# Optimization experiments

Hardware: AMD Instinct MI355X
Metric: run time of the kernel (lower is better)

## Reference

```python
import jax, jax.numpy as jnp
import numpy as np

V, E, H, NLAB, NL = 30000, 512, 256, 20, 2
B, T = 32, 512


def setup_inputs() -> dict:
    key = jax.random.key(0)
    ks = jax.random.split(key, 11)
    s = 0.05
    return {
        "input": jax.random.randint(ks[0], (B, T), 0, V, dtype=jnp.int32),
        "mask": jnp.ones((B, T), dtype=bool),
        "embed_table": jax.random.normal(ks[1], (V, E), jnp.float32) * s,
        "Wih": jax.random.normal(ks[2], (NL, 2, 4 * H, E), jnp.float32) * s,  # layer input dim E == 2H
        "Whh": jax.random.normal(ks[3], (NL, 2, 4 * H, H), jnp.float32) * s,
        "bias": jax.random.normal(ks[4], (NL, 2, 4 * H), jnp.float32) * s,  # b_ih + b_hh fused
        "lin_W": jax.random.normal(ks[5], (NLAB, 2 * H), jnp.float32) * s,
        "lin_b": jax.random.normal(ks[6], (NLAB,), jnp.float32) * s,
        "transitions": jax.random.normal(ks[7], (NLAB, NLAB), jnp.float32) * 0.1,
        "start_trans": jax.random.normal(ks[8], (NLAB,), jnp.float32) * 0.1,
        "end_trans": jax.random.normal(ks[9], (NLAB,), jnp.float32) * 0.1,
    }


def _lstm_dir(x, Wih, Whh, b, reverse):
    # x: [B,T,in] -> hs: [B,T,H]
    pre = jnp.swapaxes(x, 0, 1) @ Wih.T + b  # [T,B,4H] input projection precomputed
    h0 = jnp.zeros((x.shape[0], Whh.shape[1]), x.dtype)

    def step(carry, p):
        h, c = carry
        g = p + h @ Whh.T
        i, f, gg, o = jnp.split(g, 4, axis=-1)  # pytorch gate order i,f,g,o
        i = jax.nn.sigmoid(i); f = jax.nn.sigmoid(f)
        gg = jnp.tanh(gg); o = jax.nn.sigmoid(o)
        c = f * c + i * gg
        h = o * jnp.tanh(c)
        return (h, c), h

    _, hs = jax.lax.scan(step, (h0, h0), pre, reverse=reverse)
    return jnp.swapaxes(hs, 0, 1)


def _bilstm(x, Wih, Whh, bias):
    out = x
    for l in range(Wih.shape[0]):
        f = _lstm_dir(out, Wih[l, 0], Whh[l, 0], bias[l, 0], False)
        bwd = _lstm_dir(out, Wih[l, 1], Whh[l, 1], bias[l, 1], True)
        out = jnp.concatenate([f, bwd], axis=-1)
    return out


def _viterbi(em, mask, trans, start, end):
    # em: [B,T,L], mask: [B,T] (mask[:,0] assumed all True, as torchcrf requires)
    Bz, Tz, Lz = em.shape
    ar = jnp.arange(Lz, dtype=jnp.int32)
    score0 = start[None, :] + em[:, 0]

    def step(score, xs):
        em_t, m_t = xs  # [B,L], [B]
        ns = score[:, :, None] + trans[None] + em_t[:, None, :]  # [B,L_prev,L_cur]
        best = ns.max(axis=1)
        idx = ns.argmax(axis=1).astype(jnp.int32)
        score = jnp.where(m_t[:, None], best, score)
        idx = jnp.where(m_t[:, None], idx, ar[None, :])  # identity bp for padded steps
        return score, idx

    em_tb = jnp.swapaxes(em, 0, 1)
    m_tb = jnp.swapaxes(mask, 0, 1)
    score, hist = jax.lax.scan(step, score0, (em_tb[1:], m_tb[1:]))
    score = score + end[None, :]
    last = jnp.argmax(score, axis=-1).astype(jnp.int32)
    bidx = jnp.arange(Bz)

    def back(tag, bp):
        prev = bp[bidx, tag]
        return prev, prev

    _, prevs = jax.lax.scan(back, last, hist, reverse=True)  # prevs[t] = tag_t for t=0..T-2
    tags = jnp.concatenate([prevs, last[None]], axis=0)  # [T,B]
    return jnp.swapaxes(tags, 0, 1), score.max(axis=-1)


def reference(input, mask, embed_table, Wih, Whh, bias, lin_W, lin_b, transitions, start_trans, end_trans):
    x = embed_table[input]                      # [B,T,E]
    h = _bilstm(x, Wih, Whh, bias)              # [B,T,2H]
    em = h @ lin_W.T + lin_b                    # [B,T,L]
    tags, _ = _viterbi(em, mask, transitions, start_trans, end_trans)
    return tags
```

## Files before the change

### kernel.cpp

```cpp
#include <hip/hip_runtime.h>
#include <math.h>


#define T_SEQ   512
#define BATCH   32
#define HID     256
#define NLAB    20

#define AGENT __HIP_MEMORY_SCOPE_AGENT
#define HB_STRIDE 576
#define HB_LAYER  (64 * HB_STRIDE)

__device__ __forceinline__ float fsig(float x) {
  float e = __builtin_amdgcn_exp2f(-1.44269504088896340736f * x);
  return __builtin_amdgcn_rcpf(1.f + e);
}
__device__ __forceinline__ float ftanh(float x) {
  float e = __builtin_amdgcn_exp2f(2.88539008177792681471f * x);
  return 1.f - 2.f * __builtin_amdgcn_rcpf(e + 1.f);
}
__device__ __forceinline__ float addx1(float x) {
  int p = __builtin_amdgcn_update_dpp(0, __float_as_int(x), 0xB1, 0xF, 0xF, true);
  return x + __int_as_float(p);
}
__device__ __forceinline__ float addx2(float x) {
  int p = __builtin_amdgcn_update_dpp(0, __float_as_int(x), 0x4E, 0xF, 0xF, true);
  return x + __int_as_float(p);
}
__device__ __forceinline__ float addx4h(float x) {
  int p = __builtin_amdgcn_update_dpp(0, __float_as_int(x), 0x141, 0xF, 0xF, true);
  return x + __int_as_float(p);
}

__device__ __forceinline__ void store_l2(unsigned long long* p, unsigned long long v) {
  asm volatile("global_store_dwordx2 %0, %1, off" :: "v"(p), "v"(v) : "memory");
}
__device__ __forceinline__ unsigned long long load_l2(const unsigned long long* p) {
  unsigned long long v;
  asm volatile("global_load_dwordx2 %0, %1, off sc0\n\ts_waitcnt vmcnt(0)"
               : "=v"(v) : "v"(p) : "memory");
  return v;
}

__global__ __launch_bounds__(256) void prep_wih_k(const float* __restrict__ Wih,
                                                  const float* __restrict__ bias,
                                                  float* __restrict__ Wp,
                                                  float* __restrict__ bpp) {
  int idx = blockIdx.x * 256 + threadIdx.x;
  int k4 = idx & 127;
  int n  = (idx >> 7) & 1023;
  int ld = idx >> 17;
  int q = n & 3, j = n >> 2;
  int src = ld * 1024 + q * 256 + j;
  ((float4*)Wp)[idx] = ((const float4*)Wih)[(size_t)src * 128 + k4];
  if (k4 == 0) bpp[ld * 1024 + n] = bias[src];
}

__global__ __launch_bounds__(256) void prep_whh_reg_k(const float* __restrict__ Whh,
                                                      float4* __restrict__ Wreg) {
  int idx = blockIdx.x * 256 + threadIdx.x;
  int t  = idx & 511;
  int i  = (idx >> 9) & 31;
  int bx = (idx >> 14) & 3;
  int ld = idx >> 16;
  int u = bx * 64 + (t >> 3);
  int q = i >> 3, c = i & 7;
  int k = (t & 7) * 32 + c * 4;
  Wreg[idx] = ((const float4*)Whh)[((size_t)(ld * 1024 + q * 256 + u) * 256 + k) >> 2];
}

__global__ __launch_bounds__(256) void zero_hbuf_k(int4* __restrict__ p) {
  p[blockIdx.x * 256 + threadIdx.x] = int4{0, 0, 0, 0};
}

__global__ __launch_bounds__(256) void embed_k(const int* __restrict__ inp,
                                               const float* __restrict__ tab,
                                               float* __restrict__ x) {
  int idx = blockIdx.x * 256 + threadIdx.x;
  int row = idx >> 7, c = idx & 127;
  int tok = inp[row];
  ((float4*)x)[idx] = ((const float4*)tab)[(size_t)tok * 128 + c];
}

#define GBM 128
#define GBN 128
#define GBK 32
__global__ __launch_bounds__(256) void gemm_nt_k(const float* __restrict__ A,
                                                 const float* __restrict__ W,
                                                 const float* __restrict__ bias,
                                                 float* __restrict__ C,
                                                 int M, int N, int K) {
  __shared__ float As[GBK][GBM];
  __shared__ float Ws[GBK][GBN];
  int tid = threadIdx.x;
  int bm = blockIdx.x, bn = blockIdx.y;
  int tm = (tid & 15) * 8, tn = (tid >> 4) * 8;
  int r  = tid >> 1;
  int kq = (tid & 1) * 16;
  const float* Ap = A + (size_t)(bm * GBM + r) * K + kq;
  const float* Wq = W + (size_t)(bn * GBN + r) * K + kq;

  float acc[8][8] = {};
  float4 av[4], wv[4];

#pragma unroll
  for (int j = 0; j < 4; ++j) {
    av[j] = *(const float4*)(Ap + 4 * j);
    wv[j] = *(const float4*)(Wq + 4 * j);
  }

  for (int k0 = 0; k0 < K; k0 += GBK) {
    __syncthreads();
#pragma unroll
    for (int j = 0; j < 4; ++j) {
      float ta[4], tw[4];
      *(float4*)ta = av[j]; *(float4*)tw = wv[j];
#pragma unroll
      for (int e = 0; e < 4; ++e) {
        As[kq + 4 * j + e][r] = ta[e];
        Ws[kq + 4 * j + e][r] = tw[e];
      }
    }
    __syncthreads();
    if (k0 + GBK < K) {
#pragma unroll
      for (int j = 0; j < 4; ++j) {
        av[j] = *(const float4*)(Ap + k0 + GBK + 4 * j);
        wv[j] = *(const float4*)(Wq + k0 + GBK + 4 * j);
      }
    }
#pragma unroll
    for (int kk = 0; kk < GBK; ++kk) {
      float a8[8], b8[8];
      *(float4*)&a8[0] = *(const float4*)&As[kk][tm];
      *(float4*)&a8[4] = *(const float4*)&As[kk][tm + 4];
      *(float4*)&b8[0] = *(const float4*)&Ws[kk][tn];
      *(float4*)&b8[4] = *(const float4*)&Ws[kk][tn + 4];
#pragma unroll
      for (int i = 0; i < 8; ++i)
#pragma unroll
        for (int j = 0; j < 8; ++j)
          acc[i][j] = fmaf(a8[i], b8[j], acc[i][j]);
    }
  }

  int m0 = bm * GBM + tm, n0 = bn * GBN + tn;
  float4 bv0 = *(const float4*)(bias + n0);
  float4 bv1 = *(const float4*)(bias + n0 + 4);
#pragma unroll
  for (int i = 0; i < 8; ++i) {
    float4 o0, o1;
    o0.x = acc[i][0] + bv0.x; o0.y = acc[i][1] + bv0.y;
    o0.z = acc[i][2] + bv0.z; o0.w = acc[i][3] + bv0.w;
    o1.x = acc[i][4] + bv1.x; o1.y = acc[i][5] + bv1.y;
    o1.z = acc[i][6] + bv1.z; o1.w = acc[i][7] + bv1.w;
    *(float4*)&C[(size_t)(m0 + i) * N + n0]     = o0;
    *(float4*)&C[(size_t)(m0 + i) * N + n0 + 4] = o1;
  }
}

__global__ __launch_bounds__(512, 1) void lstm_group_k(const float* __restrict__ pre,
                                                       const float4* __restrict__ WregL,
                                                       unsigned long long* __restrict__ hbufA,
                                                       unsigned long long* __restrict__ hbufB,
                                                       float* __restrict__ Hout) {
  int raw = blockIdx.x;
  int xcd = raw & 7, slot = raw >> 3;
  int g  = xcd * 8 + (slot >> 2);
  int bx = slot & 3;
  int b = g >> 1, d = g & 1;
  int tid = threadIdx.x;
  int kq = tid & 7;
  int uu = tid >> 3;
  int u  = bx * 64 + uu;
  bool lead = (kq == 0);

  __shared__ __align__(16) float hout_s[T_SEQ * 64];
  __shared__ __align__(16) float h_s[2][8 * 36];

  float4 w[32];
  const float4* wp = WregL + ((size_t)(d * 4 + bx) * 32) * 512 + tid;
#pragma unroll
  for (int i = 0; i < 32; ++i) w[i] = wp[i * 512];

  unsigned long long* hbA = hbufA + (size_t)g * HB_STRIDE;
  unsigned long long* hbB = hbufB + (size_t)g * HB_STRIDE;
  const float* preB = pre + (size_t)b * T_SEQ * 2048 + d * 1024 + bx * 256 + 4 * uu;

  float c = 0.f;

  {
    int t = d ? (T_SEQ - 1) : 0;
    float4 g4 = *(const float4*)(preB + (size_t)t * 2048);
    float iv = fsig(g4.x), fv = fsig(g4.y);
    float zv = ftanh(g4.z), ov = fsig(g4.w);
    c = fv * c + iv * zv;
    float hn = ov * ftanh(c);
    if (lead) {
      unsigned long long pv = (1ULL << 32) | (unsigned long long)__float_as_uint(hn);
      store_l2(&hbA[256 + u], pv);
      __hip_atomic_store(&hbB[256 + u], pv, __ATOMIC_RELAXED, AGENT);
      hout_s[t * 64 + uu] = hn;
    }
  }

  for (int s = 1; s < T_SEQ; ++s) {
    int t = d ? (T_SEQ - 1 - s) : s;
    float4 p4 = *(const float4*)(preB + (size_t)t * 2048);

    if (tid < 256) {
      unsigned long long* pa = &hbA[(s & 1) * 256 + tid];
      unsigned long long* pb = &hbB[(s & 1) * 256 + tid];
      unsigned long long v;
      bool got = false;
      for (int tries = 0; tries < 6; ++tries) {
        v = load_l2(pa);
        if (__all((unsigned)(v >> 32) == (unsigned)s)) { got = true; break; }
      }
      if (!got) {
        for (;;) {
          v = __hip_atomic_load(pb, __ATOMIC_RELAXED, AGENT);
          if (__all((unsigned)(v >> 32) == (unsigned)s)) break;
          __builtin_amdgcn_s_sleep(1);
        }
      }
      h_s[s & 1][(tid >> 5) * 36 + (tid & 31)] = __uint_as_float((unsigned)v);
    }
    __syncthreads();

    const float* hk = &h_s[s & 1][kq * 36];
    float4 a0 = {0.f, 0.f, 0.f, 0.f}, a1 = a0, a2 = a0, a3 = a0;
#pragma unroll
    for (int c8 = 0; c8 < 8; ++c8) {
      float4 h4 = *(const float4*)(hk + 4 * c8);
      a0.x = fmaf(w[c8].x,      h4.x, a0.x); a0.y = fmaf(w[c8].y,      h4.y, a0.y);
      a0.z = fmaf(w[c8].z,      h4.z, a0.z); a0.w = fmaf(w[c8].w,      h4.w, a0.w);
      a1.x = fmaf(w[8 + c8].x,  h4.x, a1.x); a1.y = fmaf(w[8 + c8].y,  h4.y, a1.y);
      a1.z = fmaf(w[8 + c8].z,  h4.z, a1.z); a1.w = fmaf(w[8 + c8].w,  h4.w, a1.w);
      a2.x = fmaf(w[16 + c8].x, h4.x, a2.x); a2.y = fmaf(w[16 + c8].y, h4.y, a2.y);
      a2.z = fmaf(w[16 + c8].z, h4.z, a2.z); a2.w = fmaf(w[16 + c8].w, h4.w, a2.w);
      a3.x = fmaf(w[24 + c8].x, h4.x, a3.x); a3.y = fmaf(w[24 + c8].y, h4.y, a3.y);
      a3.z = fmaf(w[24 + c8].z, h4.z, a3.z); a3.w = fmaf(w[24 + c8].w, h4.w, a3.w);
    }
    float gi = (a0.x + a0.y) + (a0.z + a0.w);
    float gf = (a1.x + a1.y) + (a1.z + a1.w);
    float gg = (a2.x + a2.y) + (a2.z + a2.w);
    float go = (a3.x + a3.y) + (a3.z + a3.w);
    gi = addx4h(addx2(addx1(gi))) + p4.x;
    gf = addx4h(addx2(addx1(gf))) + p4.y;
    gg = addx4h(addx2(addx1(gg))) + p4.z;
    go = addx4h(addx2(addx1(go))) + p4.w;

    float iv = fsig(gi), fv = fsig(gf);
    float zv = ftanh(gg), ov = fsig(go);
    c = fv * c + iv * zv;
    float hn = ov * ftanh(c);

    if (lead) {
      if (s < T_SEQ - 1) {
        unsigned long long pv = ((unsigned long long)(unsigned)(s + 1) << 32) |
                                (unsigned long long)__float_as_uint(hn);
        store_l2(&hbA[((s + 1) & 1) * 256 + u], pv);
        __hip_atomic_store(&hbB[((s + 1) & 1) * 256 + u], pv, __ATOMIC_RELAXED, AGENT);
      }
      hout_s[t * 64 + uu] = hn;
    }
  }

  __syncthreads();
  const float4* src = (const float4*)hout_s;
  float4* dst = (float4*)Hout;
#pragma unroll
  for (int i = 0; i < 16; ++i) {
    int idx = i * 512 + tid;
    int t = idx >> 4, c4 = idx & 15;
    dst[((size_t)(b * T_SEQ + t) << 7) + d * 64 + bx * 16 + c4] = src[idx];
  }
}

__global__ __launch_bounds__(256) void linear20_k(const float* __restrict__ H,
                                                  const float* __restrict__ LW,
                                                  const float* __restrict__ lb,
                                                  float* __restrict__ em) {
  __shared__ float hs[8 * 516];
  __shared__ float lws[20 * 516];
  int tid = threadIdx.x;
  int m0 = blockIdx.x * 8;
  const float4* Hp = (const float4*)(H + (size_t)m0 * 512);
  for (int v = tid; v < 1024; v += 256) {
    int rr = v >> 7, cc = v & 127;
    *(float4*)&hs[rr * 516 + cc * 4] = Hp[v];
  }
  for (int v = tid; v < 2560; v += 256) {
    int ll = v >> 7, cc = v & 127;
    *(float4*)&lws[ll * 516 + cc * 4] = ((const float4*)LW)[v];
  }
  __syncthreads();
  if (tid < 160) {
    int rr = tid / 20, ll = tid % 20;
    float acc = 0.f;
    const float* hp = &hs[rr * 516];
    const float* wp = &lws[ll * 516];
#pragma unroll 8
    for (int k = 0; k < 512; ++k) acc += hp[k] * wp[k];
    em[(size_t)(m0 + rr) * 20 + ll] = acc + lb[ll];
  }
}

__global__ __launch_bounds__(640) void viterbi_k(const float* __restrict__ em,
                                                 const float* __restrict__ trans,
                                                 const float* __restrict__ startt,
                                                 const float* __restrict__ endt,
                                                 int* __restrict__ tags) {
  __shared__ float em_s[T_SEQ * NLAB];
  __shared__ float trans_s[NLAB * NLAB];
  __shared__ float score_s[NLAB];
  __shared__ unsigned char bp[(T_SEQ - 1) * NLAB];
  int b = blockIdx.x, tid = threadIdx.x;
  const float4* emb = (const float4*)(em + (size_t)b * T_SEQ * NLAB);
  for (int v = tid; v < T_SEQ * NLAB / 4; v += 640) ((float4*)em_s)[v] = emb[v];
  for (int v = tid; v < NLAB * NLAB; v += 640) trans_s[v] = trans[v];
  if (tid < NLAB) score_s[tid] = startt[tid] + em[(size_t)b * T_SEQ * NLAB + tid];
  __syncthreads();
  int j = tid >> 5;
  int i = tid & 31;
  float tr = (i < NLAB) ? trans_s[i * NLAB + j] : -1e30f;
  for (int t = 1; t < T_SEQ; ++t) {
    float v = (i < NLAB) ? (score_s[i] + tr) : -1e30f;
    int bi = i;
#pragma unroll
    for (int off = 16; off > 0; off >>= 1) {
      float ov = __shfl_down(v, off, 32);
      int oi = __shfl_down(bi, off, 32);
      if (ov > v || (ov == v && oi < bi)) { v = ov; bi = oi; }
    }
    __syncthreads();
    if (i == 0) {
      score_s[j] = v + em_s[t * NLAB + j];
      bp[(t - 1) * NLAB + j] = (unsigned char)bi;
    }
    __syncthreads();
  }
  if (tid == 0) {
    float best = score_s[0] + endt[0]; int cur = 0;
    for (int l = 1; l < NLAB; ++l) {
      float sv = score_s[l] + endt[l];
      if (sv > best) { best = sv; cur = l; }
    }
    int* tb = tags + b * T_SEQ;
    tb[T_SEQ - 1] = cur;
    for (int s2 = T_SEQ - 2; s2 >= 0; --s2) { cur = bp[s2 * NLAB + cur]; tb[s2] = cur; }
  }
}

extern "C" void kernel_launch(void* const* d_in, const int* in_sizes, int n_in,
                              void* d_out, int out_size, void* d_ws, size_t ws_size,
                              hipStream_t stream) {
  const int*   inp   = (const int*)d_in[0];
  const float* tab   = (const float*)d_in[2];
  const float* Wih   = (const float*)d_in[3];
  const float* Whh   = (const float*)d_in[4];
  const float* bias  = (const float*)d_in[5];
  const float* linW  = (const float*)d_in[6];
  const float* linb  = (const float*)d_in[7];
  const float* trans = (const float*)d_in[8];
  const float* stt   = (const float*)d_in[9];
  const float* endt  = (const float*)d_in[10];
  int* tags = (int*)d_out;

  float* ws   = (float*)d_ws;
  float* Wp   = ws;
  float* Wreg = Wp + 2097152;
  float* bpp  = Wreg + 1048576;
  float* x    = bpp + 4096;
  float* H0   = x + 8388608;
  float* pre  = H0 + 8388608;
  float* em   = pre + 33554432;
  unsigned long long* hbufA = (unsigned long long*)em;
  unsigned long long* hbufB = hbufA + 2 * HB_LAYER;

  const float4* WregF4 = (const float4*)Wreg;

  hipLaunchKernelGGL(zero_hbuf_k, dim3(288), dim3(256), 0, stream, (int4*)hbufA);
  hipLaunchKernelGGL(prep_wih_k, dim3(2048), dim3(256), 0, stream, Wih, bias, Wp, bpp);
  hipLaunchKernelGGL(prep_whh_reg_k, dim3(1024), dim3(256), 0, stream, Whh, (float4*)Wreg);
  hipLaunchKernelGGL(embed_k, dim3(8192), dim3(256), 0, stream, inp, tab, x);

  const int M = BATCH * T_SEQ;
  hipLaunchKernelGGL(gemm_nt_k, dim3(M / GBM, 2048 / GBN), dim3(256), 0, stream,
                     x, Wp, bpp, pre, M, 2048, 512);
  hipLaunchKernelGGL(lstm_group_k, dim3(256), dim3(512), 0, stream,
                     pre, WregF4, hbufA, hbufB, H0);
  hipLaunchKernelGGL(gemm_nt_k, dim3(M / GBM, 2048 / GBN), dim3(256), 0, stream,
                     H0, Wp + 2048 * 512, bpp + 2048, pre, M, 2048, 512);
  hipLaunchKernelGGL(lstm_group_k, dim3(256), dim3(512), 0, stream,
                     pre, WregF4 + 2 * 65536, hbufA + HB_LAYER, hbufB + HB_LAYER, x);
  hipLaunchKernelGGL(linear20_k, dim3(M / 8), dim3(256), 0, stream, x, linW, linb, em);
  hipLaunchKernelGGL(viterbi_k, dim3(BATCH), dim3(640), 0, stream, em, trans, stt, endt, tags);
}
```

Before: 2.844 ms.

## Interleave forward and backward LSTM directions within each workgroup

Each workgroup now handles 32 hidden units for both directions of one batch element, where before it handled 64 units of a single direction. It keeps both directions' recurrent weights in registers and alternates polling and compute between them, so one direction's cross-workgroup h exchange latency can overlap with the other's matvec. The reduction now spans 16 lanes and the Whh register layout is reorganised to match. The risk is two barriers per step instead of one, plus serialised polling that may not actually hide latency.

```diff
diff --git a/kernel.cpp b/kernel.cpp
--- a/kernel.cpp
+++ b/kernel.cpp
@@ -29,6 +29,10 @@
 }
 __device__ __forceinline__ float addx4h(float x) {
   int p = __builtin_amdgcn_update_dpp(0, __float_as_int(x), 0x141, 0xF, 0xF, true);
+  return x + __int_as_float(p);
+}
+__device__ __forceinline__ float addx8m(float x) {
+  int p = __builtin_amdgcn_update_dpp(0, __float_as_int(x), 0x140, 0xF, 0xF, true);
   return x + __int_as_float(p);
 }
 
@@ -40,6 +44,28 @@
   asm volatile("global_load_dwordx2 %0, %1, off sc0\n\ts_waitcnt vmcnt(0)"
                : "=v"(v) : "v"(p) : "memory");
   return v;
+}
+__device__ __forceinline__ unsigned long long poll_u64(unsigned long long* fast,
+                                                       unsigned long long* slow,
+                                                       unsigned s) {
+  unsigned long long v;
+  for (int tries = 0; tries < 6; ++tries) {
+    v = load_l2(fast);
+    if (__all((unsigned)(v >> 32) == s)) return v;
+  }
+  for (;;) {
+    v = __hip_atomic_load(slow, __ATOMIC_RELAXED, AGENT);
+    if (__all((unsigned)(v >> 32) == s)) return v;
+    __builtin_amdgcn_s_sleep(1);
+  }
+}
+__device__ __forceinline__ float gdot(const float4* w, int q,
+                                      float4 h0, float4 h1, float4 h2, float4 h3) {
+  float ax = fmaf(w[q*4+0].x, h0.x, fmaf(w[q*4+1].x, h1.x, fmaf(w[q*4+2].x, h2.x, w[q*4+3].x * h3.x)));
+  float ay = fmaf(w[q*4+0].y, h0.y, fmaf(w[q*4+1].y, h1.y, fmaf(w[q*4+2].y, h2.y, w[q*4+3].y * h3.y)));
+  float az = fmaf(w[q*4+0].z, h0.z, fmaf(w[q*4+1].z, h1.z, fmaf(w[q*4+2].z, h2.z, w[q*4+3].z * h3.z)));
+  float aw = fmaf(w[q*4+0].w, h0.w, fmaf(w[q*4+1].w, h1.w, fmaf(w[q*4+2].w, h2.w, w[q*4+3].w * h3.w)));
+  return (ax + ay) + (az + aw);
 }
 
 __global__ __launch_bounds__(256) void prep_wih_k(const float* __restrict__ Wih,
@@ -59,13 +85,13 @@
 __global__ __launch_bounds__(256) void prep_whh_reg_k(const float* __restrict__ Whh,
                                                       float4* __restrict__ Wreg) {
   int idx = blockIdx.x * 256 + threadIdx.x;
-  int t  = idx & 511;
-  int i  = (idx >> 9) & 31;
-  int bx = (idx >> 14) & 3;
-  int ld = idx >> 16;
-  int u = bx * 64 + (t >> 3);
-  int q = i >> 3, c = i & 7;
-  int k = (t & 7) * 32 + c * 4;
+  int t   = idx & 511;
+  int i   = (idx >> 9) & 15;
+  int ub8 = (idx >> 13) & 7;
+  int ld  = idx >> 16;
+  int u = ub8 * 32 + (t >> 4);
+  int q = i >> 2, c = i & 3;
+  int k = (t & 15) * 16 + c * 4;
   Wreg[idx] = ((const float4*)Whh)[((size_t)(ld * 1024 + q * 256 + u) * 256 + k) >> 2];
 }
 
@@ -159,111 +185,133 @@
   }
 }
 
-__global__ __launch_bounds__(512, 1) void lstm_group_k(const float* __restrict__ pre,
-                                                       const float4* __restrict__ WregL,
-                                                       unsigned long long* __restrict__ hbufA,
-                                                       unsigned long long* __restrict__ hbufB,
-                                                       float* __restrict__ Hout) {
+__global__ __launch_bounds__(512, 1) void lstm_pair_k(const float* __restrict__ pre,
+                                                      const float4* __restrict__ WregL,
+                                                      unsigned long long* __restrict__ fastb,
+                                                      unsigned long long* __restrict__ slowb,
+                                                      float* __restrict__ Hout) {
   int raw = blockIdx.x;
   int xcd = raw & 7, slot = raw >> 3;
-  int g  = xcd * 8 + (slot >> 2);
-  int bx = slot & 3;
-  int b = g >> 1, d = g & 1;
+  int p   = xcd * 4 + (slot >> 3);
+  int ub8 = slot & 7;
+  int b = p;
   int tid = threadIdx.x;
-  int kq = tid & 7;
-  int uu = tid >> 3;
-  int u  = bx * 64 + uu;
+  int kq = tid & 15;
+  int uu = tid >> 4;
+  int u  = ub8 * 32 + uu;
   bool lead = (kq == 0);
 
-  __shared__ __align__(16) float hout_s[T_SEQ * 64];
-  __shared__ __align__(16) float h_s[2][8 * 36];
-
-  float4 w[32];
-  const float4* wp = WregL + ((size_t)(d * 4 + bx) * 32) * 512 + tid;
-#pragma unroll
-  for (int i = 0; i < 32; ++i) w[i] = wp[i * 512];
-
-  unsigned long long* hbA = hbufA + (size_t)g * HB_STRIDE;
-  unsigned long long* hbB = hbufB + (size_t)g * HB_STRIDE;
-  const float* preB = pre + (size_t)b * T_SEQ * 2048 + d * 1024 + bx * 256 + 4 * uu;
-
-  float c = 0.f;
-
+  __shared__ __align__(16) float hout_s[2][T_SEQ][32];
+  __shared__ __align__(16) float h_sA[2][16 * 18];
+  __shared__ __align__(16) float h_sB[2][16 * 18];
+
+  float4 w0[16], w1[16];
   {
-    int t = d ? (T_SEQ - 1) : 0;
-    float4 g4 = *(const float4*)(preB + (size_t)t * 2048);
-    float iv = fsig(g4.x), fv = fsig(g4.y);
-    float zv = ftanh(g4.z), ov = fsig(g4.w);
-    c = fv * c + iv * zv;
-    float hn = ov * ftanh(c);
+    const float4* wp0 = WregL + (size_t)ub8 * 8192 + tid;
+    const float4* wp1 = wp0 + 65536;
+#pragma unroll
+    for (int i = 0; i < 16; ++i) { w0[i] = wp0[i * 512]; w1[i] = wp1[i * 512]; }
+  }
+
+  int gA = 2 * b, gB = 2 * b + 1;
+  unsigned long long* fA = fastb + (size_t)gA * HB_STRIDE;
+  unsigned long long* fB = fastb + (size_t)gB * HB_STRIDE;
+  unsigned long long* sA = slowb + (size_t)gA * HB_STRIDE;
+  unsigned long long* sB = slowb + (size_t)gB * HB_STRIDE;
+
+  const float* preP = pre + (size_t)b * T_SEQ * 2048 + ub8 * 128 + 4 * uu;
+
+  float cA = 0.f, cB = 0.f;
+
+  {
+    float4 g4 = *(const float4*)(preP);
+    float iv = fsig(g4.x), fv = fsig(g4.y), zv = ftanh(g4.z), ov = fsig(g4.w);
+    cA = fv * cA + iv * zv;
+    float hn = ov * ftanh(cA);
     if (lead) {
+      hout_s[0][0][uu] = hn;
       unsigned long long pv = (1ULL << 32) | (unsigned long long)__float_as_uint(hn);
-      store_l2(&hbA[256 + u], pv);
-      __hip_atomic_store(&hbB[256 + u], pv, __ATOMIC_RELAXED, AGENT);
-      hout_s[t * 64 + uu] = hn;
+      store_l2(&fA[256 + u], pv);
+      __hip_atomic_store(&sA[256 + u], pv, __ATOMIC_RELAXED, AGENT);
+    }
+    float4 g5 = *(const float4*)(preP + (size_t)(T_SEQ - 1) * 2048 + 1024);
+    float iv2 = fsig(g5.x), fv2 = fsig(g5.y), zv2 = ftanh(g5.z), ov2 = fsig(g5.w);
+    cB = fv2 * cB + iv2 * zv2;
+    float hn2 = ov2 * ftanh(cB);
+    if (lead) {
+      hout_s[1][T_SEQ - 1][uu] = hn2;
+      unsigned long long pv = (1ULL << 32) | (unsigned long long)__float_as_uint(hn2);
+      store_l2(&fB[256 + u], pv);
+      __hip_atomic_store(&sB[256 + u], pv, __ATOMIC_RELAXED, AGENT);
     }
   }
 
   for (int s = 1; s < T_SEQ; ++s) {
-    int t = d ? (T_SEQ - 1 - s) : s;
-    float4 p4 = *(const float4*)(preB + (size_t)t * 2048);
+    int tA = s, tB = T_SEQ - 1 - s;
+    int sl = s & 1;
+    float4 pA = *(const float4*)(preP + (size_t)tA * 2048);
+    float4 pB = *(const float4*)(preP + (size_t)tB * 2048 + 1024);
 
     if (tid < 256) {
-      unsigned long long* pa = &hbA[(s & 1) * 256 + tid];
-      unsigned long long* pb = &hbB[(s & 1) * 256 + tid];
-      unsigned long long v;
-      bool got = false;
-      for (int tries = 0; tries < 6; ++tries) {
-        v = load_l2(pa);
-        if (__all((unsigned)(v >> 32) == (unsigned)s)) { got = true; break; }
-      }
-      if (!got) {
-        for (;;) {
-          v = __hip_atomic_load(pb, __ATOMIC_RELAXED, AGENT);
-          if (__all((unsigned)(v >> 32) == (unsigned)s)) break;
-          __builtin_amdgcn_s_sleep(1);
+      unsigned long long v = poll_u64(&fA[sl * 256 + tid], &sA[sl * 256 + tid], (unsigned)s);
+      h_sA[sl][(tid >> 4) * 18 + (tid & 15)] = __uint_as_float((unsigned)v);
+    }
+    __syncthreads();
+    {
+      const float* hk = &h_sA[sl][kq * 18];
+      float4 h0 = *(const float4*)hk,       h1 = *(const float4*)(hk + 4),
+             h2 = *(const float4*)(hk + 8), h3 = *(const float4*)(hk + 12);
+      float gi = gdot(w0, 0, h0, h1, h2, h3);
+      float gf = gdot(w0, 1, h0, h1, h2, h3);
+      float gg = gdot(w0, 2, h0, h1, h2, h3);
+      float go = gdot(w0, 3, h0, h1, h2, h3);
+      gi = addx8m(addx4h(addx2(addx1(gi)))) + pA.x;
+      gf = addx8m(addx4h(addx2(addx1(gf)))) + pA.y;
+      gg = addx8m(addx4h(addx2(addx1(gg)))) + pA.z;
+      go = addx8m(addx4h(addx2(addx1(go)))) + pA.w;
+      float iv = fsig(gi), fv = fsig(gf), zv = ftanh(gg), ov = fsig(go);
+      cA = fv * cA + iv * zv;
+      float hn = ov * ftanh(cA);
+      if (lead) {
+        hout_s[0][tA][uu] = hn;
+        if (s < T_SEQ - 1) {
+          unsigned long long pv = ((unsigned long long)(unsigned)(s + 1) << 32) |
+                                  (unsigned long long)__float_as_uint(hn);
+          store_l2(&fA[((s + 1) & 1) * 256 + u], pv);
+          __hip_atomic_store(&sA[((s + 1) & 1) * 256 + u], pv, __ATOMIC_RELAXED, AGENT);
         }
       }
-      h_s[s & 1][(tid >> 5) * 36 + (tid & 31)] = __uint_as_float((unsigned)v);
-    }
-    __syncthreads();
-
-    const float* hk = &h_s[s & 1][kq * 36];
-    float4 a0 = {0.f, 0.f, 0.f, 0.f}, a1 = a0, a2 = a0, a3 = a0;
-#pragma unroll
-    for (int c8 = 0; c8 < 8; ++c8) {
-      float4 h4 = *(const float4*)(hk + 4 * c8);
-      a0.x = fmaf(w[c8].x,      h4.x, a0.x); a0.y = fmaf(w[c8].y,      h4.y, a0.y);
-      a0.z = fmaf(w[c8].z,      h4.z, a0.z); a0.w = fmaf(w[c8].w,      h4.w, a0.w);
-      a1.x = fmaf(w[8 + c8].x,  h4.x, a1.x); a1.y = fmaf(w[8 + c8].y,  h4.y, a1.y);
-      a1.z = fmaf(w[8 + c8].z,  h4.z, a1.z); a1.w = fmaf(w[8 + c8].w,  h4.w, a1.w);
-      a2.x = fmaf(w[16 + c8].x, h4.x, a2.x); a2.y = fmaf(w[16 + c8].y, h4.y, a2.y);
-      a2.z = fmaf(w[16 + c8].z, h4.z, a2.z); a2.w = fmaf(w[16 + c8].w, h4.w, a2.w);
-      a3.x = fmaf(w[24 + c8].x, h4.x, a3.x); a3.y = fmaf(w[24 + c8].y, h4.y, a3.y);
-      a3.z = fmaf(w[24 + c8].z, h4.z, a3.z); a3.w = fmaf(w[24 + c8].w, h4.w, a3.w);
-    }
-    float gi = (a0.x + a0.y) + (a0.z + a0.w);
-    float gf = (a1.x + a1.y) + (a1.z + a1.w);
-    float gg = (a2.x + a2.y) + (a2.z + a2.w);
-    float go = (a3.x + a3.y) + (a3.z + a3.w);
-    gi = addx4h(addx2(addx1(gi))) + p4.x;
-    gf = addx4h(addx2(addx1(gf))) + p4.y;
-    gg = addx4h(addx2(addx1(gg))) + p4.z;
-    go = addx4h(addx2(addx1(go))) + p4.w;
-
-    float iv = fsig(gi), fv = fsig(gf);
-    float zv = ftanh(gg), ov = fsig(go);
-    c = fv * c + iv * zv;
-    float hn = ov * ftanh(c);
-
-    if (lead) {
-      if (s < T_SEQ - 1) {
-        unsigned long long pv = ((unsigned long long)(unsigned)(s + 1) << 32) |
-                                (unsigned long long)__float_as_uint(hn);
-        store_l2(&hbA[((s + 1) & 1) * 256 + u], pv);
-        __hip_atomic_store(&hbB[((s + 1) & 1) * 256 + u], pv, __ATOMIC_RELAXED, AGENT);
+    }
+
+    if (tid < 256) {
+      unsigned long long v = poll_u64(&fB[sl * 256 + tid], &sB[sl * 256 + tid], (unsigned)s);
+      h_sB[sl][(tid >> 4) * 18 + (tid & 15)] = __uint_as_float((unsigned)v);
+    }
+    __syncthreads();
+    {
+      const float* hk = &h_sB[sl][kq * 18];
+      float4 h0 = *(const float4*)hk,       h1 = *(const float4*)(hk + 4),
+             h2 = *(const float4*)(hk + 8), h3 = *(const float4*)(hk + 12);
+      float gi = gdot(w1, 0, h0, h1, h2, h3);
+      float gf = gdot(w1, 1, h0, h1, h2, h3);
+      float gg = gdot(w1, 2, h0, h1, h2, h3);
+      float go = gdot(w1, 3, h0, h1, h2, h3);
+      gi = addx8m(addx4h(addx2(addx1(gi)))) + pB.x;
+      gf = addx8m(addx4h(addx2(addx1(gf)))) + pB.y;
+      gg = addx8m(addx4h(addx2(addx1(gg)))) + pB.z;
+      go = addx8m(addx4h(addx2(addx1(go)))) + pB.w;
+      float iv = fsig(gi), fv = fsig(gf), zv = ftanh(gg), ov = fsig(go);
+      cB = fv * cB + iv * zv;
+      float hn = ov * ftanh(cB);
+      if (lead) {
+        hout_s[1][tB][uu] = hn;
+        if (s < T_SEQ - 1) {
+          unsigned long long pv = ((unsigned long long)(unsigned)(s + 1) << 32) |
+                                  (unsigned long long)__float_as_uint(hn);
+          store_l2(&fB[((s + 1) & 1) * 256 + u], pv);
+          __hip_atomic_store(&sB[((s + 1) & 1) * 256 + u], pv, __ATOMIC_RELAXED, AGENT);
+        }
       }
-      hout_s[t * 64 + uu] = hn;
     }
   }
 
@@ -273,8 +321,10 @@
 #pragma unroll
   for (int i = 0; i < 16; ++i) {
     int idx = i * 512 + tid;
-    int t = idx >> 4, c4 = idx & 15;
-    dst[((size_t)(b * T_SEQ + t) << 7) + d * 64 + bx * 16 + c4] = src[idx];
+    int d = idx >> 12;
+    int rem = idx & 4095;
+    int t = rem >> 3, c4 = rem & 7;
+    dst[((size_t)(b * T_SEQ + t) << 7) + d * 64 + ub8 * 8 + c4] = src[idx];
   }
 }
 
@@ -376,12 +426,12 @@
   float* H0   = x + 8388608;
   float* pre  = H0 + 8388608;
   float* em   = pre + 33554432;
-  unsigned long long* hbufA = (unsigned long long*)em;
-  unsigned long long* hbufB = hbufA + 2 * HB_LAYER;
+  unsigned long long* fastb = (unsigned long long*)em;
+  unsigned long long* slowb = fastb + 2 * HB_LAYER;
 
   const float4* WregF4 = (const float4*)Wreg;
 
-  hipLaunchKernelGGL(zero_hbuf_k, dim3(288), dim3(256), 0, stream, (int4*)hbufA);
+  hipLaunchKernelGGL(zero_hbuf_k, dim3(288), dim3(256), 0, stream, (int4*)fastb);
   hipLaunchKernelGGL(prep_wih_k, dim3(2048), dim3(256), 0, stream, Wih, bias, Wp, bpp);
   hipLaunchKernelGGL(prep_whh_reg_k, dim3(1024), dim3(256), 0, stream, Whh, (float4*)Wreg);
   hipLaunchKernelGGL(embed_k, dim3(8192), dim3(256), 0, stream, inp, tab, x);
@@ -389,12 +439,12 @@
   const int M = BATCH * T_SEQ;
   hipLaunchKernelGGL(gemm_nt_k, dim3(M / GBM, 2048 / GBN), dim3(256), 0, stream,
                      x, Wp, bpp, pre, M, 2048, 512);
-  hipLaunchKernelGGL(lstm_group_k, dim3(256), dim3(512), 0, stream,
-                     pre, WregF4, hbufA, hbufB, H0);
+  hipLaunchKernelGGL(lstm_pair_k, dim3(256), dim3(512), 0, stream,
+                     pre, WregF4, fastb, slowb, H0);
   hipLaunchKernelGGL(gemm_nt_k, dim3(M / GBM, 2048 / GBN), dim3(256), 0, stream,
                      H0, Wp + 2048 * 512, bpp + 2048, pre, M, 2048, 512);
-  hipLaunchKernelGGL(lstm_group_k, dim3(256), dim3(512), 0, stream,
-                     pre, WregF4 + 2 * 65536, hbufA + HB_LAYER, hbufB + HB_LAYER, x);
+  hipLaunchKernelGGL(lstm_pair_k, dim3(256), dim3(512), 0, stream,
+                     pre, WregF4 + 131072, fastb + HB_LAYER, slowb + HB_LAYER, x);
   hipLaunchKernelGGL(linear20_k, dim3(M / 8), dim3(256), 0, stream, x, linW, linb, em);
   hipLaunchKernelGGL(viterbi_k, dim3(BATCH), dim3(640), 0, stream, em, trans, stt, endt, tags);
 }
```

After: 5.258 ms. 1.85x slower.

## Enlarge GEMM tile to 256x128 and prefetch next-step preactivations in LSTM

Applied to the files above, without the earlier changes.

The input-projection GEMM tile grows from 128x128 to 256x128, with each thread computing 16x8 outputs. Shared memory gets padded strides and coalesced row-wise global loads, which raises arithmetic intensity per shared load. Separately, the LSTM recurrence loads the next timestep's precomputed gate inputs one step ahead, taking that global load latency off the serial per-step critical path. The bigger tile uses more registers and halves the grid in M, which may reduce occupancy.

```diff
diff --git a/kernel.cpp b/kernel.cpp
--- a/kernel.cpp
+++ b/kernel.cpp
@@ -82,81 +82,101 @@
   ((float4*)x)[idx] = ((const float4*)tab)[(size_t)tok * 128 + c];
 }
 
-#define GBM 128
+#define GBM 256
 #define GBN 128
 #define GBK 32
-__global__ __launch_bounds__(256) void gemm_nt_k(const float* __restrict__ A,
-                                                 const float* __restrict__ W,
-                                                 const float* __restrict__ bias,
-                                                 float* __restrict__ C,
-                                                 int M, int N, int K) {
-  __shared__ float As[GBK][GBM];
-  __shared__ float Ws[GBK][GBN];
+#define LDA 258
+#define LDB 130
+__global__ __launch_bounds__(256, 2) void gemm_nt_k(const float* __restrict__ A,
+                                                    const float* __restrict__ W,
+                                                    const float* __restrict__ bias,
+                                                    float* __restrict__ C,
+                                                    int M, int N, int K) {
+  __shared__ float As[GBK * LDA];
+  __shared__ float Ws[GBK * LDB];
   int tid = threadIdx.x;
   int bm = blockIdx.x, bn = blockIdx.y;
-  int tm = (tid & 15) * 8, tn = (tid >> 4) * 8;
-  int r  = tid >> 1;
-  int kq = (tid & 1) * 16;
-  const float* Ap = A + (size_t)(bm * GBM + r) * K + kq;
-  const float* Wq = W + (size_t)(bn * GBN + r) * K + kq;
-
-  float acc[8][8] = {};
-  float4 av[4], wv[4];
-
-#pragma unroll
-  for (int j = 0; j < 4; ++j) {
-    av[j] = *(const float4*)(Ap + 4 * j);
-    wv[j] = *(const float4*)(Wq + 4 * j);
+  int tm = (tid & 15) * 4;
+  int tn = (tid >> 4) * 8;
+  const float* Ap = A + (size_t)(bm * GBM) * K;
+  const float* Wq = W + (size_t)(bn * GBN) * K;
+
+  float acc[16][8] = {};
+  float4 avr[8], wvr[4];
+
+#pragma unroll
+  for (int i = 0; i < 8; ++i) {
+    int v = i * 256 + tid;
+    avr[i] = *(const float4*)(Ap + (size_t)(v >> 3) * K + (v & 7) * 4);
+  }
+#pragma unroll
+  for (int i = 0; i < 4; ++i) {
+    int v = i * 256 + tid;
+    wvr[i] = *(const float4*)(Wq + (size_t)(v >> 3) * K + (v & 7) * 4);
   }
 
   for (int k0 = 0; k0 < K; k0 += GBK) {
     __syncthreads();
 #pragma unroll
-    for (int j = 0; j < 4; ++j) {
-      float ta[4], tw[4];
-      *(float4*)ta = av[j]; *(float4*)tw = wv[j];
-#pragma unroll
-      for (int e = 0; e < 4; ++e) {
-        As[kq + 4 * j + e][r] = ta[e];
-        Ws[kq + 4 * j + e][r] = tw[e];
-      }
+    for (int i = 0; i < 8; ++i) {
+      int v = i * 256 + tid, r = v >> 3, kc = (v & 7) * 4;
+      float tmp[4]; *(float4*)tmp = avr[i];
+#pragma unroll
+      for (int e = 0; e < 4; ++e) As[(kc + e) * LDA + r] = tmp[e];
+    }
+#pragma unroll
+    for (int i = 0; i < 4; ++i) {
+      int v = i * 256 + tid, r = v >> 3, kc = (v & 7) * 4;
+      float tmp[4]; *(float4*)tmp = wvr[i];
+#pragma unroll
+      for (int e = 0; e < 4; ++e) Ws[(kc + e) * LDB + r] = tmp[e];
     }
     __syncthreads();
     if (k0 + GBK < K) {
 #pragma unroll
-      for (int j = 0; j < 4; ++j) {
-        av[j] = *(const float4*)(Ap + k0 + GBK + 4 * j);
-        wv[j] = *(const float4*)(Wq + k0 + GBK + 4 * j);
+      for (int i = 0; i < 8; ++i) {
+        int v = i * 256 + tid;
+        avr[i] = *(const float4*)(Ap + (size_t)(v >> 3) * K + k0 + GBK + (v & 7) * 4);
       }
+#pragma unroll
+      for (int i = 0; i < 4; ++i) {
+        int v = i * 256 + tid;
+        wvr[i] = *(const float4*)(Wq + (size_t)(v >> 3) * K + k0 + GBK + (v & 7) * 4);
+      }
     }
 #pragma unroll
     for (int kk = 0; kk < GBK; ++kk) {
-      float a8[8], b8[8];
-      *(float4*)&a8[0] = *(const float4*)&As[kk][tm];
-      *(float4*)&a8[4] = *(const float4*)&As[kk][tm + 4];
-      *(float4*)&b8[0] = *(const float4*)&Ws[kk][tn];
-      *(float4*)&b8[4] = *(const float4*)&Ws[kk][tn + 4];
-#pragma unroll
-      for (int i = 0; i < 8; ++i)
+      float a16[16], b8[8];
+#pragma unroll
+      for (int g = 0; g < 4; ++g)
+        *(float4*)&a16[4 * g] = *(const float4*)&As[kk * LDA + tm + 64 * g];
+      *(float4*)&b8[0] = *(const float4*)&Ws[kk * LDB + tn];
+      *(float4*)&b8[4] = *(const float4*)&Ws[kk * LDB + tn + 4];
+#pragma unroll
+      for (int i = 0; i < 16; ++i)
 #pragma unroll
         for (int j = 0; j < 8; ++j)
-          acc[i][j] = fmaf(a8[i], b8[j], acc[i][j]);
-    }
-  }
-
-  int m0 = bm * GBM + tm, n0 = bn * GBN + tn;
+          acc[i][j] = fmaf(a16[i], b8[j], acc[i][j]);
+    }
+  }
+
+  int n0 = bn * GBN + tn;
   float4 bv0 = *(const float4*)(bias + n0);
   float4 bv1 = *(const float4*)(bias + n0 + 4);
 #pragma unroll
-  for (int i = 0; i < 8; ++i) {
-    float4 o0, o1;
-    o0.x = acc[i][0] + bv0.x; o0.y = acc[i][1] + bv0.y;
-    o0.z = acc[i][2] + bv0.z; o0.w = acc[i][3] + bv0.w;
-    o1.x = acc[i][4] + bv1.x; o1.y = acc[i][5] + bv1.y;
-    o1.z = acc[i][6] + bv1.z; o1.w = acc[i][7] + bv1.w;
-    *(float4*)&C[(size_t)(m0 + i) * N + n0]     = o0;
-    *(float4*)&C[(size_t)(m0 + i) * N + n0 + 4] = o1;
-  }
+  for (int g = 0; g < 4; ++g)
+#pragma unroll
+    for (int e = 0; e < 4; ++e) {
+      int i = g * 4 + e;
+      int row = bm * GBM + tm + 64 * g + e;
+      float4 o0, o1;
+      o0.x = acc[i][0] + bv0.x; o0.y = acc[i][1] + bv0.y;
+      o0.z = acc[i][2] + bv0.z; o0.w = acc[i][3] + bv0.w;
+      o1.x = acc[i][4] + bv1.x; o1.y = acc[i][5] + bv1.y;
+      o1.z = acc[i][6] + bv1.z; o1.w = acc[i][7] + bv1.w;
+      *(float4*)&C[(size_t)row * N + n0]     = o0;
+      *(float4*)&C[(size_t)row * N + n0 + 4] = o1;
+    }
 }
 
 __global__ __launch_bounds__(512, 1) void lstm_group_k(const float* __restrict__ pre,
@@ -204,9 +224,10 @@
     }
   }
 
+  float4 p_cur = *(const float4*)(preB + (size_t)(d ? (T_SEQ - 2) : 1) * 2048);
+
   for (int s = 1; s < T_SEQ; ++s) {
     int t = d ? (T_SEQ - 1 - s) : s;
-    float4 p4 = *(const float4*)(preB + (size_t)t * 2048);
 
     if (tid < 256) {
       unsigned long long* pa = &hbA[(s & 1) * 256 + tid];
@@ -228,6 +249,9 @@
     }
     __syncthreads();
 
+    int snx = (s + 1 < T_SEQ) ? s + 1 : s;
+    float4 p_nxt = *(const float4*)(preB + (size_t)(d ? (T_SEQ - 1 - snx) : snx) * 2048);
+
     const float* hk = &h_s[s & 1][kq * 36];
     float4 a0 = {0.f, 0.f, 0.f, 0.f}, a1 = a0, a2 = a0, a3 = a0;
 #pragma unroll
@@ -246,10 +270,10 @@
     float gf = (a1.x + a1.y) + (a1.z + a1.w);
     float gg = (a2.x + a2.y) + (a2.z + a2.w);
     float go = (a3.x + a3.y) + (a3.z + a3.w);
-    gi = addx4h(addx2(addx1(gi))) + p4.x;
-    gf = addx4h(addx2(addx1(gf))) + p4.y;
-    gg = addx4h(addx2(addx1(gg))) + p4.z;
-    go = addx4h(addx2(addx1(go))) + p4.w;
+    gi = addx4h(addx2(addx1(gi))) + p_cur.x;
+    gf = addx4h(addx2(addx1(gf))) + p_cur.y;
+    gg = addx4h(addx2(addx1(gg))) + p_cur.z;
+    go = addx4h(addx2(addx1(go))) + p_cur.w;
 
     float iv = fsig(gi), fv = fsig(gf);
     float zv = ftanh(gg), ov = fsig(go);
@@ -265,6 +289,7 @@
       }
       hout_s[t * 64 + uu] = hn;
     }
+    p_cur = p_nxt;
   }
 
   __syncthreads();
```

New measurement: 2.872 ms. No clear change (+1.0%).
